# Performance work log

Hardware: AMD Instinct MI355X
Metric: run time of the kernel (lower is better)

## Reference

```python
import jax, jax.numpy as jnp
import numpy as np

REG = 0.01          # regularisation (target epsilon)
DECAY = 0.9         # decay_rate
MIN_UPDATE = 0.01   # min_update_size
MAX_ITERS = 50      # max_iterations
GRAD_CLIP = 1.0     # transport_gradient_clip
B, N, D = 4, 2048, 16


@jax.custom_vjp
def clip_grad_identity(t):
    # identity fwd; clips the cotangent of the transport matrix in bwd
    return t

def _cg_fwd(t):
    return t, None

def _cg_bwd(_, dt):
    return (jnp.clip(dt, -GRAD_CLIP, GRAD_CLIP),)

clip_grad_identity.defvjp(_cg_fwd, _cg_bwd)


def _diameter(x):
    # max over dims of per-sample std (ddof=0), per batch -> (B,1)
    d = jnp.max(jnp.std(x, axis=1), axis=-1, keepdims=True)
    return jnp.where(d == 0.0, jnp.ones_like(d), d)


def _sq_cdist(x):
    # squared euclidean auto-distance matrix, (B,N,N)
    sq = jnp.sum(x * x, axis=-1)
    c = sq[:, :, None] + sq[:, None, :] - 2.0 * jnp.einsum('bnd,bmd->bnm', x, x)
    return jnp.maximum(c, 0.0)


def sinkhorn_loop(log_a, log_b, cost, eps_target, min_update, max_iter, eps0, rate):
    """Log-domain Sinkhorn with per-batch exponentially decayed epsilon and
    masked early stopping (data-dependent stop expressed as a convergence mask
    so the loop is jit/vjp friendly). eps0: (B,1,1) initial regularisation
    (extent of the scaled particles, per Thornton & Corenflos)."""
    Bb, _ = log_a.shape
    init = (jnp.zeros_like(log_a), jnp.zeros_like(log_b), eps0,
            jnp.zeros((Bb, 1), dtype=bool))

    @jax.checkpoint
    def step(carry, _):
        f, g, eps, done = carry              # eps: (B,1,1), done: (B,1)
        eps2 = eps[:, :, 0]                  # (B,1)
        # f_i = -eps * LSE_j( log_b_j + (g_j - C_ij)/eps )
        f_new = -eps2 * jax.nn.logsumexp(log_b[:, None, :] + (g[:, None, :] - cost) / eps, axis=-1)
        cT = jnp.swapaxes(cost, 1, 2)
        # g_j = -eps * LSE_i( log_a_i + (f_i - C_ij)/eps )
        g_new = -eps2 * jax.nn.logsumexp(log_a[:, None, :] + (f_new[:, None, :] - cT) / eps, axis=-1)
        upd = jnp.maximum(jnp.max(jnp.abs(f_new - f), axis=-1),
                          jnp.max(jnp.abs(g_new - g), axis=-1))[:, None]  # (B,1)
        converged = (upd < min_update) & (eps2 <= eps_target)
        f = jnp.where(done, f, f_new)
        g = jnp.where(done, g, g_new)
        eps = jnp.where(done[:, :, None], eps, jnp.maximum(eps * rate, eps_target))
        done = done | converged
        return (f, g, eps, done), None

    (f, g, eps, _), _ = jax.lax.scan(step, init, None, length=max_iter)
    return f, g, eps


def _forward(state, weight):
    n = state.shape[1]
    log_b = jnp.full(weight.shape, -jnp.log(float(n)), weight.dtype)  # log uniform
    centred = state - jax.lax.stop_gradient(jnp.mean(state, axis=1, keepdims=True))
    scale = jax.lax.stop_gradient(_diameter(state)) * jnp.sqrt(float(state.shape[-1]))  # (B,1)
    sx = centred / scale[:, :, None]
    cost = _sq_cdist(sx)                                              # (B,N,N)
    extent = (jnp.max(sx, axis=(1, 2)) - jnp.min(sx, axis=(1, 2))).reshape(-1, 1, 1)
    f, g, _ = sinkhorn_loop(weight, log_b, cost, REG, MIN_UPDATE, MAX_ITERS, extent, DECAY)
    # transport from potentials at the target regularisation
    log_T = weight[:, :, None] + log_b[:, None, :] + (f[:, :, None] + g[:, None, :] - cost) / REG
    transport = clip_grad_identity(jnp.exp(log_T))                    # (B,N,N)
    # new particle m = N * sum_n T_nm x_n
    new_state = float(n) * jnp.einsum('bnm,bnd->bmd', transport, state)
    return new_state


def setup_inputs() -> dict:
    key = jax.random.key(0)
    k1, k2 = jax.random.split(key)
    state = jax.random.normal(k1, (B, N, D), dtype=jnp.float32)
    weight = jax.nn.log_softmax(jax.random.normal(k2, (B, N), dtype=jnp.float32), axis=-1)
    return {"state": state, "weight": weight}


def reference(state, weight):
    new_state = _forward(state, weight)
    uniform_log_w = jnp.full(weight.shape, -jnp.log(float(weight.shape[1])), weight.dtype)
    return (new_state, uniform_log_w)
```

## Files before the change

kernel.cpp:

```cpp
#include <hip/hip_runtime.h>

#define BATCH 4
#define NPTS  2048
#define DIM   16
#define REGEPS 0.01f
#define DECAYF 0.9f
#define MINUPD 0.01f
#define MAXIT  50
#define LOGN   7.62461898616f
#define L2E    1.44269504089f
#define LN2    0.69314718056f

#define OFF_SX    0
#define OFF_SQ    (BATCH*NPTS*DIM)
#define OFF_F     (OFF_SQ + BATCH*NPTS)
#define OFF_G     (OFF_F + BATCH*NPTS)
#define OFF_MEAN  (OFF_G + BATCH*NPTS)
#define OFF_SCALE (OFF_MEAN + BATCH*DIM)
#define OFF_EPS0  (OFF_SCALE + BATCH)
#define OFF_SYNC  155776

__global__ __launch_bounds__(256) void ot_preproc(const float* __restrict__ state,
                                                  float* __restrict__ ws) {
  const int b = blockIdx.x;
  const int tid = threadIdx.x;
  __shared__ float s_sum[16][17];
  __shared__ float s_sq[16][17];
  __shared__ float s_mean[16];
  __shared__ float s_red[8];
  __shared__ float s_scale_sh;

  const float* st = state + b * NPTS * DIM;
  const int d = tid & 15, grp = tid >> 4;
  float sm = 0.f, s2 = 0.f;
  for (int n = grp; n < NPTS; n += 16) {
    float x = st[n * DIM + d];
    sm += x; s2 += x * x;
  }
  s_sum[grp][d] = sm; s_sq[grp][d] = s2;
  __syncthreads();
  if (tid < 16) {
    float S = 0.f, Q = 0.f;
    for (int g2 = 0; g2 < 16; ++g2) { S += s_sum[g2][tid]; Q += s_sq[g2][tid]; }
    float mean = S * (1.0f / NPTS);
    float var  = fmaxf(Q * (1.0f / NPTS) - mean * mean, 0.f);
    float sd   = sqrtf(var);
    s_mean[tid] = mean;
    ws[OFF_MEAN + b * DIM + tid] = mean;
    s_sum[0][tid] = sd;
  }
  __syncthreads();
  if (tid == 0) {
    float dm = 0.f;
    for (int d2 = 0; d2 < 16; ++d2) dm = fmaxf(dm, s_sum[0][d2]);
    if (dm == 0.f) dm = 1.f;
    float scale = dm * 4.0f;
    s_scale_sh = scale;
    ws[OFF_SCALE + b] = scale;
  }
  __syncthreads();

  const float inv_scale = 1.0f / s_scale_sh;
  float vmin = 3.0e38f, vmax = -3.0e38f;
  float* sx = ws + OFF_SX + b * NPTS * DIM;
  float* sq = ws + OFF_SQ + b * NPTS;
  for (int n = tid; n < NPTS; n += 256) {
    const float4* rp = (const float4*)(st + n * DIM);
    float4 xs0 = rp[0], xs1 = rp[1], xs2 = rp[2], xs3 = rp[3];
    float xv[16] = {xs0.x,xs0.y,xs0.z,xs0.w, xs1.x,xs1.y,xs1.z,xs1.w,
                    xs2.x,xs2.y,xs2.z,xs2.w, xs3.x,xs3.y,xs3.z,xs3.w};
    float ov[16];
    float q = 0.f;
    #pragma unroll
    for (int e = 0; e < 16; ++e) {
      float v = (xv[e] - s_mean[e]) * inv_scale;
      ov[e] = v; q += v * v;
      vmin = fminf(vmin, v); vmax = fmaxf(vmax, v);
    }
    float4* op = (float4*)(sx + n * DIM);
    op[0] = make_float4(ov[0],ov[1],ov[2],ov[3]);
    op[1] = make_float4(ov[4],ov[5],ov[6],ov[7]);
    op[2] = make_float4(ov[8],ov[9],ov[10],ov[11]);
    op[3] = make_float4(ov[12],ov[13],ov[14],ov[15]);
    sq[n] = q;
  }
  float* fv = ws + OFF_F + b * NPTS;
  float* gv = ws + OFF_G + b * NPTS;
  for (int n = tid; n < NPTS; n += 256) { fv[n] = 0.f; gv[n] = 0.f; }
  #pragma unroll
  for (int off = 32; off > 0; off >>= 1) {
    vmin = fminf(vmin, __shfl_xor(vmin, off));
    vmax = fmaxf(vmax, __shfl_xor(vmax, off));
  }
  const int wv = tid >> 6, ln = tid & 63;
  if (ln == 0) { s_red[wv] = vmin; s_red[4 + wv] = vmax; }
  __syncthreads();
  if (tid == 0) {
    float mn = fminf(fminf(s_red[0], s_red[1]), fminf(s_red[2], s_red[3]));
    float mx = fmaxf(fmaxf(s_red[4], s_red[5]), fmaxf(s_red[6], s_red[7]));
    ws[OFF_EPS0 + b] = mx - mn;
    int* sy = (int*)ws + OFF_SYNC + b * 64;
    sy[0] = 0;
    ((unsigned int*)sy)[2] = 0u;
    ((unsigned int*)sy)[3] = 0u;
    sy[32] = 0;
  }
}

__device__ __forceinline__ float4 load_f4_coherent(const float* p) {
  float4 v;
  asm volatile("global_load_dwordx4 %0, %1, off sc0 sc1\n\t"
               "s_waitcnt vmcnt(0)"
               : "=v"(v) : "v"(p) : "memory");
  return v;
}

__device__ __forceinline__ void batch_barrier(int* sy, int ph) {
  __syncthreads();
  if (threadIdx.x == 0) {
    int* arrive = sy;
    int* epoch  = sy + 32;
    const int old = __hip_atomic_fetch_add(arrive, 1, __ATOMIC_ACQ_REL,
                                           __HIP_MEMORY_SCOPE_AGENT);
    if (old == 64 * ph - 1) {
      __hip_atomic_store(epoch, ph, __ATOMIC_RELEASE, __HIP_MEMORY_SCOPE_AGENT);
    } else {
      while (__hip_atomic_load(epoch, __ATOMIC_RELAXED, __HIP_MEMORY_SCOPE_AGENT) < ph)
        __builtin_amdgcn_s_sleep(2);
      (void)__hip_atomic_load(epoch, __ATOMIC_ACQUIRE, __HIP_MEMORY_SCOPE_AGENT);
    }
  }
  __syncthreads();
}

__device__ __forceinline__ void lse_sweep(const float* __restrict__ s_xt,
                                          const float* __restrict__ s_a2,
                                          const float (&sxs)[4][16],
                                          float (&M)[4], float (&S)[4], int l) {
  #pragma unroll
  for (int r = 0; r < 4; ++r) { M[r] = -3.0e38f; S[r] = 0.0f; }
  for (int c = 0; c < 8; ++c) {
    const int jb = c * 256 + 4 * l;
    const float4 av = *(const float4*)(s_a2 + jb);
    float acc[4][4];
    {
      const float4 xj = *(const float4*)(s_xt + jb);
      #pragma unroll
      for (int r = 0; r < 4; ++r) {
        acc[r][0] = fmaf(sxs[r][0], xj.x, av.x);
        acc[r][1] = fmaf(sxs[r][0], xj.y, av.y);
        acc[r][2] = fmaf(sxs[r][0], xj.z, av.z);
        acc[r][3] = fmaf(sxs[r][0], xj.w, av.w);
      }
    }
    #pragma unroll
    for (int dd = 1; dd < 16; ++dd) {
      const float4 xj = *(const float4*)(s_xt + dd * 2048 + jb);
      #pragma unroll
      for (int r = 0; r < 4; ++r) {
        acc[r][0] = fmaf(sxs[r][dd], xj.x, acc[r][0]);
        acc[r][1] = fmaf(sxs[r][dd], xj.y, acc[r][1]);
        acc[r][2] = fmaf(sxs[r][dd], xj.z, acc[r][2]);
        acc[r][3] = fmaf(sxs[r][dd], xj.w, acc[r][3]);
      }
    }
    #pragma unroll
    for (int r = 0; r < 4; ++r) {
      const float cmx = fmaxf(fmaxf(acc[r][0], acc[r][1]), fmaxf(acc[r][2], acc[r][3]));
      const float nm = fmaxf(M[r], cmx);
      const float e0 = exp2f(M[r] - nm);
      const float sa = exp2f(acc[r][0]-nm) + exp2f(acc[r][1]-nm)
                     + exp2f(acc[r][2]-nm) + exp2f(acc[r][3]-nm);
      S[r] = fmaf(S[r], e0, sa);
      M[r] = nm;
    }
  }
}

__device__ __forceinline__ void lse_butterfly(float (&M)[4], float (&S)[4]) {
  #pragma unroll
  for (int off = 1; off < 64; off <<= 1) {
    #pragma unroll
    for (int r = 0; r < 4; ++r) {
      const float om = __shfl_xor(M[r], off);
      const float os = __shfl_xor(S[r], off);
      const float nm = fmaxf(M[r], om);
      S[r] = S[r] * exp2f(M[r] - nm) + os * exp2f(om - nm);
      M[r] = nm;
    }
  }
}

__global__ __launch_bounds__(512, 2) void ot_sinkhorn(float* __restrict__ ws,
                                                      const float* __restrict__ wlog) {
  extern __shared__ float lds[];
  float* s_xt  = lds;
  float* s_a2  = lds + 16 * 2048;
  float* s_wl2 = s_a2 + 2048;

  const int bid = blockIdx.x;
  const int b  = bid >> 6;
  const int rb = bid & 63;
  const int tid = threadIdx.x;
  const int w = tid >> 6, l = tid & 63;

  const float* __restrict__ sx = ws + OFF_SX + b * NPTS * DIM;
  const float* __restrict__ sq = ws + OFF_SQ + b * NPTS;
  float* fv = ws + OFF_F + b * NPTS;
  float* gv = ws + OFF_G + b * NPTS;
  const float* __restrict__ wl = wlog + b * NPTS;
  int* sy = (int*)ws + OFF_SYNC + b * 64;
  unsigned int* up2 = (unsigned int*)sy + 2;

  for (int j = tid; j < NPTS; j += 512) {
    const float4* rp = (const float4*)(sx + j * DIM);
    float4 t0 = rp[0], t1 = rp[1], t2 = rp[2], t3 = rp[3];
    s_xt[ 0*2048+j]=t0.x; s_xt[ 1*2048+j]=t0.y; s_xt[ 2*2048+j]=t0.z; s_xt[ 3*2048+j]=t0.w;
    s_xt[ 4*2048+j]=t1.x; s_xt[ 5*2048+j]=t1.y; s_xt[ 6*2048+j]=t1.z; s_xt[ 7*2048+j]=t1.w;
    s_xt[ 8*2048+j]=t2.x; s_xt[ 9*2048+j]=t2.y; s_xt[10*2048+j]=t2.z; s_xt[11*2048+j]=t2.w;
    s_xt[12*2048+j]=t3.x; s_xt[13*2048+j]=t3.y; s_xt[14*2048+j]=t3.z; s_xt[15*2048+j]=t3.w;
    s_wl2[j] = wl[j] * L2E;
  }
  const int row0 = rb * 32 + w * 4;
  float sxs[4][16];
  #pragma unroll
  for (int r = 0; r < 4; ++r) {
    const float4* rp = (const float4*)(sx + (row0 + r) * DIM);
    float4 t0 = rp[0], t1 = rp[1], t2 = rp[2], t3 = rp[3];
    sxs[r][0]=t0.x;  sxs[r][1]=t0.y;  sxs[r][2]=t0.z;  sxs[r][3]=t0.w;
    sxs[r][4]=t1.x;  sxs[r][5]=t1.y;  sxs[r][6]=t1.z;  sxs[r][7]=t1.w;
    sxs[r][8]=t2.x;  sxs[r][9]=t2.y;  sxs[r][10]=t2.z; sxs[r][11]=t2.w;
    sxs[r][12]=t3.x; sxs[r][13]=t3.y; sxs[r][14]=t3.z; sxs[r][15]=t3.w;
  }
  float eps = ws[OFF_EPS0 + b];
  {
    const float s2e0 = 2.0f * L2E / eps;
    #pragma unroll
    for (int r = 0; r < 4; ++r)
      #pragma unroll
      for (int dd = 0; dd < 16; ++dd) sxs[r][dd] *= s2e0;
  }
  __syncthreads();

  int ph = 0;
  for (int it = 0; it < MAXIT; ++it) {
    const float le   = L2E / eps;
    const float eln2 = eps * LN2;

    {
      const int j4 = tid * 4;
      const float4 gj = load_f4_coherent(gv + j4);
      const float4 qj = *(const float4*)(sq + j4);
      *(float4*)(s_a2 + j4) = make_float4((gj.x - qj.x) * le, (gj.y - qj.y) * le,
                                          (gj.z - qj.z) * le, (gj.w - qj.w) * le);
    }
    __syncthreads();
    {
      float M[4], S[4];
      lse_sweep(s_xt, s_a2, sxs, M, S, l);
      lse_butterfly(M, S);
      if (l < 4) {
        const float Mr = (l==0)?M[0]:(l==1)?M[1]:(l==2)?M[2]:M[3];
        const float Sr = (l==0)?S[0]:(l==1)?S[1]:(l==2)?S[2]:S[3];
        const int i = row0 + l;
        const float qi = sq[i];
        const float fnew = fmaf(eps, LOGN, qi) - eln2 * (Mr + log2f(Sr));
        const float old = __hip_atomic_load(fv + i, __ATOMIC_RELAXED, __HIP_MEMORY_SCOPE_AGENT);
        __hip_atomic_store(fv + i, fnew, __ATOMIC_RELEASE, __HIP_MEMORY_SCOPE_AGENT);
        __hip_atomic_fetch_max(up2 + (it & 1), __float_as_uint(fabsf(fnew - old)),
                               __ATOMIC_RELAXED, __HIP_MEMORY_SCOPE_AGENT);
      }
    }
    ++ph; batch_barrier(sy, ph);

    if (rb == 0 && tid == 0)
      __hip_atomic_store(up2 + ((it + 1) & 1), 0u, __ATOMIC_RELAXED, __HIP_MEMORY_SCOPE_AGENT);
    {
      const int j4 = tid * 4;
      const float4 fj = load_f4_coherent(fv + j4);
      const float4 qj = *(const float4*)(sq + j4);
      const float4 w2 = *(const float4*)(s_wl2 + j4);
      *(float4*)(s_a2 + j4) = make_float4(fmaf(fj.x - qj.x, le, w2.x), fmaf(fj.y - qj.y, le, w2.y),
                                          fmaf(fj.z - qj.z, le, w2.z), fmaf(fj.w - qj.w, le, w2.w));
    }
    __syncthreads();
    {
      float M[4], S[4];
      lse_sweep(s_xt, s_a2, sxs, M, S, l);
      lse_butterfly(M, S);
      if (l < 4) {
        const float Mr = (l==0)?M[0]:(l==1)?M[1]:(l==2)?M[2]:M[3];
        const float Sr = (l==0)?S[0]:(l==1)?S[1]:(l==2)?S[2]:S[3];
        const int i = row0 + l;
        const float qm = sq[i];
        const float gnew = qm - eln2 * (Mr + log2f(Sr));
        const float old = __hip_atomic_load(gv + i, __ATOMIC_RELAXED, __HIP_MEMORY_SCOPE_AGENT);
        __hip_atomic_store(gv + i, gnew, __ATOMIC_RELEASE, __HIP_MEMORY_SCOPE_AGENT);
        __hip_atomic_fetch_max(up2 + (it & 1), __float_as_uint(fabsf(gnew - old)),
                               __ATOMIC_RELAXED, __HIP_MEMORY_SCOPE_AGENT);
      }
    }
    if (it < MAXIT - 1) {
      ++ph; batch_barrier(sy, ph);
      const unsigned uu = __hip_atomic_load(up2 + (it & 1), __ATOMIC_RELAXED, __HIP_MEMORY_SCOPE_AGENT);
      const bool conv = (__uint_as_float(uu) < MINUPD) && (eps <= REGEPS);
      if (conv) break;
      const float en = fmaxf(eps * DECAYF, REGEPS);
      const float ratio = eps / en;
      eps = en;
      #pragma unroll
      for (int r = 0; r < 4; ++r)
        #pragma unroll
        for (int dd = 0; dd < 16; ++dd) sxs[r][dd] *= ratio;
    }
  }
}

__global__ __launch_bounds__(256) void ot_out(float* __restrict__ ws,
                                              const float* __restrict__ wlog,
                                              float* __restrict__ out) {
  __shared__ float s_xt[DIM][256];
  __shared__ float s_p[256];
  __shared__ float s_q[256];
  const int bid = blockIdx.x;
  const int b  = bid >> 8;
  const int rb = bid & 255;
  const int tid = threadIdx.x;
  const int w = tid >> 6, l = tid & 63;
  const float invR = 1.0f / REGEPS;

  const float* __restrict__ sx = ws + OFF_SX + b * NPTS * DIM;
  const float* __restrict__ sq = ws + OFF_SQ + b * NPTS;
  const float* __restrict__ fv = ws + OFF_F + b * NPTS;
  const float* __restrict__ gv = ws + OFF_G + b * NPTS;
  const float* __restrict__ wl = wlog + b * NPTS;

  const int row0 = rb * 8 + w * 2;
  float sxm[2][DIM], cm2[2], qm[2], acc[2][DIM], accT[2];
  #pragma unroll
  for (int r = 0; r < 2; ++r) {
    const int mrow = row0 + r;
    cm2[r] = sq[mrow];
    qm[r]  = gv[mrow] * invR;
    const float4* rp = (const float4*)(sx + mrow * DIM);
    #pragma unroll
    for (int c4 = 0; c4 < 4; ++c4) {
      float4 t = rp[c4];
      sxm[r][c4*4+0] = -2.0f * t.x; sxm[r][c4*4+1] = -2.0f * t.y;
      sxm[r][c4*4+2] = -2.0f * t.z; sxm[r][c4*4+3] = -2.0f * t.w;
    }
    #pragma unroll
    for (int dd = 0; dd < DIM; ++dd) acc[r][dd] = 0.0f;
    accT[r] = 0.0f;
  }

  for (int k = 0; k < NPTS / 256; ++k) {
    __syncthreads();
    {
      const int n = k * 256 + tid;
      const float4* rp = (const float4*)(sx + n * DIM);
      float4 t0 = rp[0], t1 = rp[1], t2 = rp[2], t3 = rp[3];
      s_xt[0][tid]=t0.x;  s_xt[1][tid]=t0.y;  s_xt[2][tid]=t0.z;  s_xt[3][tid]=t0.w;
      s_xt[4][tid]=t1.x;  s_xt[5][tid]=t1.y;  s_xt[6][tid]=t1.z;  s_xt[7][tid]=t1.w;
      s_xt[8][tid]=t2.x;  s_xt[9][tid]=t2.y;  s_xt[10][tid]=t2.z; s_xt[11][tid]=t2.w;
      s_xt[12][tid]=t3.x; s_xt[13][tid]=t3.y; s_xt[14][tid]=t3.z; s_xt[15][tid]=t3.w;
      s_q[tid] = sq[n];
      s_p[tid] = wl[n] - LOGN + fv[n] * invR;
    }
    __syncthreads();
    const float4 pv = *(const float4*)&s_p[4 * l];
    const float4 qv = *(const float4*)&s_q[4 * l];
    float a2[2][4];
    #pragma unroll
    for (int r = 0; r < 2; ++r) {
      a2[r][0] = cm2[r] + qv.x; a2[r][1] = cm2[r] + qv.y;
      a2[r][2] = cm2[r] + qv.z; a2[r][3] = cm2[r] + qv.w;
    }
    #pragma unroll
    for (int dd = 0; dd < DIM; ++dd) {
      const float4 xj = *(const float4*)&s_xt[dd][4 * l];
      #pragma unroll
      for (int r = 0; r < 2; ++r) {
        const float xr = sxm[r][dd];
        a2[r][0] = fmaf(xr, xj.x, a2[r][0]);
        a2[r][1] = fmaf(xr, xj.y, a2[r][1]);
        a2[r][2] = fmaf(xr, xj.z, a2[r][2]);
        a2[r][3] = fmaf(xr, xj.w, a2[r][3]);
      }
    }
    float T[2][4];
    #pragma unroll
    for (int r = 0; r < 2; ++r) {
      T[r][0] = __expf(fmaf(fmaxf(a2[r][0], 0.f), -invR, pv.x + qm[r]));
      T[r][1] = __expf(fmaf(fmaxf(a2[r][1], 0.f), -invR, pv.y + qm[r]));
      T[r][2] = __expf(fmaf(fmaxf(a2[r][2], 0.f), -invR, pv.z + qm[r]));
      T[r][3] = __expf(fmaf(fmaxf(a2[r][3], 0.f), -invR, pv.w + qm[r]));
      accT[r] += (T[r][0] + T[r][1]) + (T[r][2] + T[r][3]);
    }
    #pragma unroll
    for (int dd = 0; dd < DIM; ++dd) {
      const float4 xj = *(const float4*)&s_xt[dd][4 * l];
      #pragma unroll
      for (int r = 0; r < 2; ++r) {
        float t = acc[r][dd];
        t = fmaf(T[r][0], xj.x, t);
        t = fmaf(T[r][1], xj.y, t);
        t = fmaf(T[r][2], xj.z, t);
        t = fmaf(T[r][3], xj.w, t);
        acc[r][dd] = t;
      }
    }
  }
  #pragma unroll
  for (int off = 1; off < 64; off <<= 1) {
    #pragma unroll
    for (int r = 0; r < 2; ++r) {
      #pragma unroll
      for (int dd = 0; dd < DIM; ++dd) acc[r][dd] += __shfl_xor(acc[r][dd], off);
      accT[r] += __shfl_xor(accT[r], off);
    }
  }
  if (l == 0) {
    const float scale = ws[OFF_SCALE + b];
    const float* mean = ws + OFF_MEAN + b * DIM;
    #pragma unroll
    for (int r = 0; r < 2; ++r) {
      const int mrow = row0 + r;
      float ov[16];
      #pragma unroll
      for (int dd = 0; dd < DIM; ++dd)
        ov[dd] = (float)NPTS * fmaf(scale, acc[r][dd], mean[dd] * accT[r]);
      float4* op = (float4*)(out + (b * NPTS + mrow) * DIM);
      op[0] = make_float4(ov[0],ov[1],ov[2],ov[3]);
      op[1] = make_float4(ov[4],ov[5],ov[6],ov[7]);
      op[2] = make_float4(ov[8],ov[9],ov[10],ov[11]);
      op[3] = make_float4(ov[12],ov[13],ov[14],ov[15]);
    }
  }
  if (tid < 8) out[BATCH * NPTS * DIM + b * NPTS + rb * 8 + tid] = -LOGN;
}

extern "C" void kernel_launch(void* const* d_in, const int* in_sizes, int n_in,
                              void* d_out, int out_size, void* d_ws, size_t ws_size,
                              hipStream_t stream) {
  (void)in_sizes; (void)n_in; (void)out_size; (void)ws_size;
  const float* state  = (const float*)d_in[0];
  const float* weight = (const float*)d_in[1];
  float* out = (float*)d_out;
  float* ws  = (float*)d_ws;

  ot_preproc<<<dim3(BATCH), dim3(256), 0, stream>>>(state, ws);

  const unsigned int dynLds = 147456;
  hipFuncSetAttribute((const void*)ot_sinkhorn,
                      hipFuncAttributeMaxDynamicSharedMemorySize, (int)dynLds);
  hipLaunchKernelGGL(ot_sinkhorn, dim3(256), dim3(512), dynLds, stream, ws, weight);

  ot_out<<<dim3(BATCH * NPTS / 8), dim3(256), 0, stream>>>(ws, weight, out);
}
```

Before: 3.311 ms.

## Split Sinkhorn LSE column sweep across two wave groups with LDS merge

Doubles the Sinkhorn block to 1024 threads so two groups of waves each sweep half of the columns for the same rows, then merges the partial max/sum pairs through a small LDS buffer. Row coordinates become wave-uniform (readfirstlane) and unscaled by epsilon, with 1/eps applied at the end of each tile instead of rescaling 64 registers per iteration. This aims to raise parallelism and latency hiding per CU, at the cost of an extra __syncthreads and merge step per half-iteration and more register pressure under the 1024-thread launch bound.

Result: no change. 3.364 ms (+1.6%).

```diff
diff --git a/kernel.cpp b/kernel.cpp
--- a/kernel.cpp
+++ b/kernel.cpp
@@ -133,24 +133,29 @@
   __syncthreads();
 }
 
-__device__ __forceinline__ void lse_sweep(const float* __restrict__ s_xt,
-                                          const float* __restrict__ s_a2,
-                                          const float (&sxs)[4][16],
-                                          float (&M)[4], float (&S)[4], int l) {
+__device__ __forceinline__ float rfl(float v) {
+  return __int_as_float(__builtin_amdgcn_readfirstlane(__float_as_int(v)));
+}
+
+__device__ __forceinline__ void lse_sweep_half(const float* __restrict__ s_xt,
+                                               const float* __restrict__ s_a2,
+                                               const float (&sxr)[4][16],
+                                               float inv_eps, int jbase, int l,
+                                               float (&M)[4], float (&S)[4]) {
   #pragma unroll
   for (int r = 0; r < 4; ++r) { M[r] = -3.0e38f; S[r] = 0.0f; }
-  for (int c = 0; c < 8; ++c) {
-    const int jb = c * 256 + 4 * l;
+  for (int c = 0; c < 4; ++c) {
+    const int jb = jbase + c * 256 + 4 * l;
     const float4 av = *(const float4*)(s_a2 + jb);
     float acc[4][4];
     {
       const float4 xj = *(const float4*)(s_xt + jb);
       #pragma unroll
       for (int r = 0; r < 4; ++r) {
-        acc[r][0] = fmaf(sxs[r][0], xj.x, av.x);
-        acc[r][1] = fmaf(sxs[r][0], xj.y, av.y);
-        acc[r][2] = fmaf(sxs[r][0], xj.z, av.z);
-        acc[r][3] = fmaf(sxs[r][0], xj.w, av.w);
+        acc[r][0] = sxr[r][0] * xj.x;
+        acc[r][1] = sxr[r][0] * xj.y;
+        acc[r][2] = sxr[r][0] * xj.z;
+        acc[r][3] = sxr[r][0] * xj.w;
       }
     }
     #pragma unroll
@@ -158,19 +163,22 @@
       const float4 xj = *(const float4*)(s_xt + dd * 2048 + jb);
       #pragma unroll
       for (int r = 0; r < 4; ++r) {
-        acc[r][0] = fmaf(sxs[r][dd], xj.x, acc[r][0]);
-        acc[r][1] = fmaf(sxs[r][dd], xj.y, acc[r][1]);
-        acc[r][2] = fmaf(sxs[r][dd], xj.z, acc[r][2]);
-        acc[r][3] = fmaf(sxs[r][dd], xj.w, acc[r][3]);
+        acc[r][0] = fmaf(sxr[r][dd], xj.x, acc[r][0]);
+        acc[r][1] = fmaf(sxr[r][dd], xj.y, acc[r][1]);
+        acc[r][2] = fmaf(sxr[r][dd], xj.z, acc[r][2]);
+        acc[r][3] = fmaf(sxr[r][dd], xj.w, acc[r][3]);
       }
     }
     #pragma unroll
     for (int r = 0; r < 4; ++r) {
-      const float cmx = fmaxf(fmaxf(acc[r][0], acc[r][1]), fmaxf(acc[r][2], acc[r][3]));
+      const float v0 = fmaf(acc[r][0], inv_eps, av.x);
+      const float v1 = fmaf(acc[r][1], inv_eps, av.y);
+      const float v2 = fmaf(acc[r][2], inv_eps, av.z);
+      const float v3 = fmaf(acc[r][3], inv_eps, av.w);
+      const float cmx = fmaxf(fmaxf(v0, v1), fmaxf(v2, v3));
       const float nm = fmaxf(M[r], cmx);
       const float e0 = exp2f(M[r] - nm);
-      const float sa = exp2f(acc[r][0]-nm) + exp2f(acc[r][1]-nm)
-                     + exp2f(acc[r][2]-nm) + exp2f(acc[r][3]-nm);
+      const float sa = exp2f(v0-nm) + exp2f(v1-nm) + exp2f(v2-nm) + exp2f(v3-nm);
       S[r] = fmaf(S[r], e0, sa);
       M[r] = nm;
     }
@@ -191,18 +199,21 @@
   }
 }
 
-__global__ __launch_bounds__(512, 2) void ot_sinkhorn(float* __restrict__ ws,
-                                                      const float* __restrict__ wlog) {
+__global__ __launch_bounds__(1024, 4) void ot_sinkhorn(float* __restrict__ ws,
+                                                       const float* __restrict__ wlog) {
   extern __shared__ float lds[];
   float* s_xt  = lds;
   float* s_a2  = lds + 16 * 2048;
   float* s_wl2 = s_a2 + 2048;
+  float* s_mrg = s_wl2 + 2048;
 
   const int bid = blockIdx.x;
   const int b  = bid >> 6;
   const int rb = bid & 63;
   const int tid = threadIdx.x;
   const int w = tid >> 6, l = tid & 63;
+  const int wlo = w & 7;
+  const int jbase = (w >> 3) * 1024;
 
   const float* __restrict__ sx = ws + OFF_SX + b * NPTS * DIM;
   const float* __restrict__ sq = ws + OFF_SQ + b * NPTS;
@@ -212,7 +223,7 @@
   int* sy = (int*)ws + OFF_SYNC + b * 64;
   unsigned int* up2 = (unsigned int*)sy + 2;
 
-  for (int j = tid; j < NPTS; j += 512) {
+  for (int j = tid; j < NPTS; j += 1024) {
     const float4* rp = (const float4*)(sx + j * DIM);
     float4 t0 = rp[0], t1 = rp[1], t2 = rp[2], t3 = rp[3];
     s_xt[ 0*2048+j]=t0.x; s_xt[ 1*2048+j]=t0.y; s_xt[ 2*2048+j]=t0.z; s_xt[ 3*2048+j]=t0.w;
@@ -221,33 +232,28 @@
     s_xt[12*2048+j]=t3.x; s_xt[13*2048+j]=t3.y; s_xt[14*2048+j]=t3.z; s_xt[15*2048+j]=t3.w;
     s_wl2[j] = wl[j] * L2E;
   }
-  const int row0 = rb * 32 + w * 4;
-  float sxs[4][16];
+  const int row0 = rb * 32 + wlo * 4;
+  float sxr[4][16];
   #pragma unroll
   for (int r = 0; r < 4; ++r) {
     const float4* rp = (const float4*)(sx + (row0 + r) * DIM);
-    float4 t0 = rp[0], t1 = rp[1], t2 = rp[2], t3 = rp[3];
-    sxs[r][0]=t0.x;  sxs[r][1]=t0.y;  sxs[r][2]=t0.z;  sxs[r][3]=t0.w;
-    sxs[r][4]=t1.x;  sxs[r][5]=t1.y;  sxs[r][6]=t1.z;  sxs[r][7]=t1.w;
-    sxs[r][8]=t2.x;  sxs[r][9]=t2.y;  sxs[r][10]=t2.z; sxs[r][11]=t2.w;
-    sxs[r][12]=t3.x; sxs[r][13]=t3.y; sxs[r][14]=t3.z; sxs[r][15]=t3.w;
+    const float4 t0 = rp[0], t1 = rp[1], t2 = rp[2], t3 = rp[3];
+    const float c2 = 2.0f * L2E;
+    sxr[r][0]=rfl(t0.x*c2);  sxr[r][1]=rfl(t0.y*c2);  sxr[r][2]=rfl(t0.z*c2);  sxr[r][3]=rfl(t0.w*c2);
+    sxr[r][4]=rfl(t1.x*c2);  sxr[r][5]=rfl(t1.y*c2);  sxr[r][6]=rfl(t1.z*c2);  sxr[r][7]=rfl(t1.w*c2);
+    sxr[r][8]=rfl(t2.x*c2);  sxr[r][9]=rfl(t2.y*c2);  sxr[r][10]=rfl(t2.z*c2); sxr[r][11]=rfl(t2.w*c2);
+    sxr[r][12]=rfl(t3.x*c2); sxr[r][13]=rfl(t3.y*c2); sxr[r][14]=rfl(t3.z*c2); sxr[r][15]=rfl(t3.w*c2);
   }
   float eps = ws[OFF_EPS0 + b];
-  {
-    const float s2e0 = 2.0f * L2E / eps;
-    #pragma unroll
-    for (int r = 0; r < 4; ++r)
-      #pragma unroll
-      for (int dd = 0; dd < 16; ++dd) sxs[r][dd] *= s2e0;
-  }
   __syncthreads();
 
   int ph = 0;
   for (int it = 0; it < MAXIT; ++it) {
-    const float le   = L2E / eps;
-    const float eln2 = eps * LN2;
-
-    {
+    const float le      = L2E / eps;
+    const float eln2    = eps * LN2;
+    const float inv_eps = 1.0f / eps;
+
+    if (tid < 512) {
       const int j4 = tid * 4;
       const float4 gj = load_f4_coherent(gv + j4);
       const float4 qj = *(const float4*)(sq + j4);
@@ -257,14 +263,25 @@
     __syncthreads();
     {
       float M[4], S[4];
-      lse_sweep(s_xt, s_a2, sxs, M, S, l);
+      lse_sweep_half(s_xt, s_a2, sxr, inv_eps, jbase, l, M, S);
       lse_butterfly(M, S);
-      if (l < 4) {
+      if (w >= 8 && l < 4) {
         const float Mr = (l==0)?M[0]:(l==1)?M[1]:(l==2)?M[2]:M[3];
         const float Sr = (l==0)?S[0]:(l==1)?S[1]:(l==2)?S[2]:S[3];
+        s_mrg[(wlo * 4 + l) * 2]     = Mr;
+        s_mrg[(wlo * 4 + l) * 2 + 1] = Sr;
+      }
+      __syncthreads();
+      if (w < 8 && l < 4) {
+        const float M1 = (l==0)?M[0]:(l==1)?M[1]:(l==2)?M[2]:M[3];
+        const float S1 = (l==0)?S[0]:(l==1)?S[1]:(l==2)?S[2]:S[3];
+        const float M2 = s_mrg[(wlo * 4 + l) * 2];
+        const float S2 = s_mrg[(wlo * 4 + l) * 2 + 1];
+        const float nm = fmaxf(M1, M2);
+        const float St = S1 * exp2f(M1 - nm) + S2 * exp2f(M2 - nm);
         const int i = row0 + l;
         const float qi = sq[i];
-        const float fnew = fmaf(eps, LOGN, qi) - eln2 * (Mr + log2f(Sr));
+        const float fnew = fmaf(eps, LOGN, qi) - eln2 * (nm + log2f(St));
         const float old = __hip_atomic_load(fv + i, __ATOMIC_RELAXED, __HIP_MEMORY_SCOPE_AGENT);
         __hip_atomic_store(fv + i, fnew, __ATOMIC_RELEASE, __HIP_MEMORY_SCOPE_AGENT);
         __hip_atomic_fetch_max(up2 + (it & 1), __float_as_uint(fabsf(fnew - old)),
@@ -275,7 +292,7 @@
 
     if (rb == 0 && tid == 0)
       __hip_atomic_store(up2 + ((it + 1) & 1), 0u, __ATOMIC_RELAXED, __HIP_MEMORY_SCOPE_AGENT);
-    {
+    if (tid < 512) {
       const int j4 = tid * 4;
       const float4 fj = load_f4_coherent(fv + j4);
       const float4 qj = *(const float4*)(sq + j4);
@@ -286,14 +303,25 @@
     __syncthreads();
     {
       float M[4], S[4];
-      lse_sweep(s_xt, s_a2, sxs, M, S, l);
+      lse_sweep_half(s_xt, s_a2, sxr, inv_eps, jbase, l, M, S);
       lse_butterfly(M, S);
-      if (l < 4) {
+      if (w >= 8 && l < 4) {
         const float Mr = (l==0)?M[0]:(l==1)?M[1]:(l==2)?M[2]:M[3];
         const float Sr = (l==0)?S[0]:(l==1)?S[1]:(l==2)?S[2]:S[3];
+        s_mrg[(wlo * 4 + l) * 2]     = Mr;
+        s_mrg[(wlo * 4 + l) * 2 + 1] = Sr;
+      }
+      __syncthreads();
+      if (w < 8 && l < 4) {
+        const float M1 = (l==0)?M[0]:(l==1)?M[1]:(l==2)?M[2]:M[3];
+        const float S1 = (l==0)?S[0]:(l==1)?S[1]:(l==2)?S[2]:S[3];
+        const float M2 = s_mrg[(wlo * 4 + l) * 2];
+        const float S2 = s_mrg[(wlo * 4 + l) * 2 + 1];
+        const float nm = fmaxf(M1, M2);
+        const float St = S1 * exp2f(M1 - nm) + S2 * exp2f(M2 - nm);
         const int i = row0 + l;
         const float qm = sq[i];
-        const float gnew = qm - eln2 * (Mr + log2f(Sr));
+        const float gnew = qm - eln2 * (nm + log2f(St));
         const float old = __hip_atomic_load(gv + i, __ATOMIC_RELAXED, __HIP_MEMORY_SCOPE_AGENT);
         __hip_atomic_store(gv + i, gnew, __ATOMIC_RELEASE, __HIP_MEMORY_SCOPE_AGENT);
         __hip_atomic_fetch_max(up2 + (it & 1), __float_as_uint(fabsf(gnew - old)),
@@ -305,13 +333,7 @@
       const unsigned uu = __hip_atomic_load(up2 + (it & 1), __ATOMIC_RELAXED, __HIP_MEMORY_SCOPE_AGENT);
       const bool conv = (__uint_as_float(uu) < MINUPD) && (eps <= REGEPS);
       if (conv) break;
-      const float en = fmaxf(eps * DECAYF, REGEPS);
-      const float ratio = eps / en;
-      eps = en;
-      #pragma unroll
-      for (int r = 0; r < 4; ++r)
-        #pragma unroll
-        for (int dd = 0; dd < 16; ++dd) sxs[r][dd] *= ratio;
+      eps = fmaxf(eps * DECAYF, REGEPS);
     }
   }
 }
@@ -451,10 +473,10 @@
 
   ot_preproc<<<dim3(BATCH), dim3(256), 0, stream>>>(state, ws);
 
-  const unsigned int dynLds = 147456;
+  const unsigned int dynLds = 147712;
   hipFuncSetAttribute((const void*)ot_sinkhorn,
                       hipFuncAttributeMaxDynamicSharedMemorySize, (int)dynLds);
-  hipLaunchKernelGGL(ot_sinkhorn, dim3(256), dim3(512), dynLds, stream, ws, weight);
+  hipLaunchKernelGGL(ot_sinkhorn, dim3(256), dim3(1024), dynLds, stream, ws, weight);
 
   ot_out<<<dim3(BATCH * NPTS / 8), dim3(256), 0, stream>>>(ws, weight, out);
 }
```

## Replace atomic-counter barrier with flag array, packed-FMA sweep, local update reduction

Applied to the files above, without the earlier changes.

Replaces the per-batch atomic fetch-add grid barrier with per-block flag stores that block 0 polls through a wavefront ballot before publishing an epoch. The convergence max is now reduced inside each block and issued as a single atomic per block rather than one per row. The row-feature registers are reloaded from LDS every iteration, and 1/eps is applied after the dot product using packed two-wide FMAs. Squared norms are cached in LDS. The aim is to shorten barrier latency and cut atomic traffic and register pressure, at the cost of extra LDS reads and a slightly different rounding order.

After: 4.316 ms. 1.3x slower.

```diff
diff --git a/kernel.cpp b/kernel.cpp
--- a/kernel.cpp
+++ b/kernel.cpp
@@ -10,6 +10,8 @@
 #define LOGN   7.62461898616f
 #define L2E    1.44269504089f
 #define LN2    0.69314718056f
+
+typedef float v2f __attribute__((ext_vector_type(2)));
 
 #define OFF_SX    0
 #define OFF_SQ    (BATCH*NPTS*DIM)
@@ -99,12 +101,9 @@
     float mn = fminf(fminf(s_red[0], s_red[1]), fminf(s_red[2], s_red[3]));
     float mx = fmaxf(fmaxf(s_red[4], s_red[5]), fmaxf(s_red[6], s_red[7]));
     ws[OFF_EPS0 + b] = mx - mn;
-    int* sy = (int*)ws + OFF_SYNC + b * 64;
-    sy[0] = 0;
-    ((unsigned int*)sy)[2] = 0u;
-    ((unsigned int*)sy)[3] = 0u;
-    sy[32] = 0;
-  }
+  }
+  int* sy = (int*)ws + OFF_SYNC + b * 128;
+  for (int k = tid; k < 128; k += 256) sy[k] = 0;
 }
 
 __device__ __forceinline__ float4 load_f4_coherent(const float* p) {
@@ -115,19 +114,25 @@
   return v;
 }
 
-__device__ __forceinline__ void batch_barrier(int* sy, int ph) {
-  __syncthreads();
-  if (threadIdx.x == 0) {
-    int* arrive = sy;
-    int* epoch  = sy + 32;
-    const int old = __hip_atomic_fetch_add(arrive, 1, __ATOMIC_ACQ_REL,
-                                           __HIP_MEMORY_SCOPE_AGENT);
-    if (old == 64 * ph - 1) {
-      __hip_atomic_store(epoch, ph, __ATOMIC_RELEASE, __HIP_MEMORY_SCOPE_AGENT);
-    } else {
+__device__ __forceinline__ void batch_barrier(int* flags, int* epoch, int rb, int ph) {
+  __syncthreads();
+  const int tid = threadIdx.x;
+  if (tid < 64) {
+    if (tid == 0)
+      __hip_atomic_store(flags + rb, ph, __ATOMIC_RELEASE, __HIP_MEMORY_SCOPE_AGENT);
+    if (rb == 0) {
+      for (;;) {
+        const int v = __hip_atomic_load(flags + tid, __ATOMIC_RELAXED, __HIP_MEMORY_SCOPE_AGENT);
+        if (__ballot(v >= ph) == 0xFFFFFFFFFFFFFFFFull) break;
+        __builtin_amdgcn_s_sleep(4);
+      }
+      __threadfence();
+      if (tid == 0)
+        __hip_atomic_store(epoch, ph, __ATOMIC_RELEASE, __HIP_MEMORY_SCOPE_AGENT);
+    } else if (tid == 0) {
       while (__hip_atomic_load(epoch, __ATOMIC_RELAXED, __HIP_MEMORY_SCOPE_AGENT) < ph)
-        __builtin_amdgcn_s_sleep(2);
-      (void)__hip_atomic_load(epoch, __ATOMIC_ACQUIRE, __HIP_MEMORY_SCOPE_AGENT);
+        __builtin_amdgcn_s_sleep(4);
+      __threadfence();
     }
   }
   __syncthreads();
@@ -135,42 +140,47 @@
 
 __device__ __forceinline__ void lse_sweep(const float* __restrict__ s_xt,
                                           const float* __restrict__ s_a2,
-                                          const float (&sxs)[4][16],
-                                          float (&M)[4], float (&S)[4], int l) {
+                                          const float (&sxr)[4][16],
+                                          float inv_eps, int l,
+                                          float (&M)[4], float (&S)[4]) {
+  const v2f inv2 = { inv_eps, inv_eps };
   #pragma unroll
   for (int r = 0; r < 4; ++r) { M[r] = -3.0e38f; S[r] = 0.0f; }
   for (int c = 0; c < 8; ++c) {
     const int jb = c * 256 + 4 * l;
-    const float4 av = *(const float4*)(s_a2 + jb);
-    float acc[4][4];
-    {
-      const float4 xj = *(const float4*)(s_xt + jb);
+    const v2f* a2v = (const v2f*)(s_a2 + jb);
+    const v2f av0 = a2v[0], av1 = a2v[1];
+    v2f acc[4][2];
+    {
+      const v2f* xv = (const v2f*)(s_xt + jb);
+      const v2f x0 = xv[0], x1 = xv[1];
       #pragma unroll
       for (int r = 0; r < 4; ++r) {
-        acc[r][0] = fmaf(sxs[r][0], xj.x, av.x);
-        acc[r][1] = fmaf(sxs[r][0], xj.y, av.y);
-        acc[r][2] = fmaf(sxs[r][0], xj.z, av.z);
-        acc[r][3] = fmaf(sxs[r][0], xj.w, av.w);
+        const v2f sv = { sxr[r][0], sxr[r][0] };
+        acc[r][0] = x0 * sv;
+        acc[r][1] = x1 * sv;
       }
     }
     #pragma unroll
     for (int dd = 1; dd < 16; ++dd) {
-      const float4 xj = *(const float4*)(s_xt + dd * 2048 + jb);
+      const v2f* xv = (const v2f*)(s_xt + dd * 2048 + jb);
+      const v2f x0 = xv[0], x1 = xv[1];
       #pragma unroll
       for (int r = 0; r < 4; ++r) {
-        acc[r][0] = fmaf(sxs[r][dd], xj.x, acc[r][0]);
-        acc[r][1] = fmaf(sxs[r][dd], xj.y, acc[r][1]);
-        acc[r][2] = fmaf(sxs[r][dd], xj.z, acc[r][2]);
-        acc[r][3] = fmaf(sxs[r][dd], xj.w, acc[r][3]);
+        const v2f sv = { sxr[r][dd], sxr[r][dd] };
+        acc[r][0] = __builtin_elementwise_fma(x0, sv, acc[r][0]);
+        acc[r][1] = __builtin_elementwise_fma(x1, sv, acc[r][1]);
       }
     }
     #pragma unroll
     for (int r = 0; r < 4; ++r) {
-      const float cmx = fmaxf(fmaxf(acc[r][0], acc[r][1]), fmaxf(acc[r][2], acc[r][3]));
+      const v2f v01 = __builtin_elementwise_fma(acc[r][0], inv2, av0);
+      const v2f v23 = __builtin_elementwise_fma(acc[r][1], inv2, av1);
+      const float v0 = v01.x, v1 = v01.y, v2 = v23.x, v3 = v23.y;
+      const float cmx = fmaxf(fmaxf(v0, v1), fmaxf(v2, v3));
       const float nm = fmaxf(M[r], cmx);
       const float e0 = exp2f(M[r] - nm);
-      const float sa = exp2f(acc[r][0]-nm) + exp2f(acc[r][1]-nm)
-                     + exp2f(acc[r][2]-nm) + exp2f(acc[r][3]-nm);
+      const float sa = exp2f(v0-nm) + exp2f(v1-nm) + exp2f(v2-nm) + exp2f(v3-nm);
       S[r] = fmaf(S[r], e0, sa);
       M[r] = nm;
     }
@@ -197,6 +207,8 @@
   float* s_xt  = lds;
   float* s_a2  = lds + 16 * 2048;
   float* s_wl2 = s_a2 + 2048;
+  float* s_q   = s_wl2 + 2048;
+  float* s_red = s_q + 2048;
 
   const int bid = blockIdx.x;
   const int b  = bid >> 6;
@@ -209,8 +221,10 @@
   float* fv = ws + OFF_F + b * NPTS;
   float* gv = ws + OFF_G + b * NPTS;
   const float* __restrict__ wl = wlog + b * NPTS;
-  int* sy = (int*)ws + OFF_SYNC + b * 64;
-  unsigned int* up2 = (unsigned int*)sy + 2;
+  int* sy    = (int*)ws + OFF_SYNC + b * 128;
+  int* flags = sy;
+  int* epoch = sy + 64;
+  unsigned int* up2 = (unsigned int*)sy + 66;
 
   for (int j = tid; j < NPTS; j += 512) {
     const float4* rp = (const float4*)(sx + j * DIM);
@@ -220,98 +234,107 @@
     s_xt[ 8*2048+j]=t2.x; s_xt[ 9*2048+j]=t2.y; s_xt[10*2048+j]=t2.z; s_xt[11*2048+j]=t2.w;
     s_xt[12*2048+j]=t3.x; s_xt[13*2048+j]=t3.y; s_xt[14*2048+j]=t3.z; s_xt[15*2048+j]=t3.w;
     s_wl2[j] = wl[j] * L2E;
+    s_q[j]   = sq[j];
   }
   const int row0 = rb * 32 + w * 4;
-  float sxs[4][16];
-  #pragma unroll
-  for (int r = 0; r < 4; ++r) {
-    const float4* rp = (const float4*)(sx + (row0 + r) * DIM);
-    float4 t0 = rp[0], t1 = rp[1], t2 = rp[2], t3 = rp[3];
-    sxs[r][0]=t0.x;  sxs[r][1]=t0.y;  sxs[r][2]=t0.z;  sxs[r][3]=t0.w;
-    sxs[r][4]=t1.x;  sxs[r][5]=t1.y;  sxs[r][6]=t1.z;  sxs[r][7]=t1.w;
-    sxs[r][8]=t2.x;  sxs[r][9]=t2.y;  sxs[r][10]=t2.z; sxs[r][11]=t2.w;
-    sxs[r][12]=t3.x; sxs[r][13]=t3.y; sxs[r][14]=t3.z; sxs[r][15]=t3.w;
-  }
+  const float qi_own = (l < 4) ? sq[row0 + l] : 0.f;
+  float fprev = 0.f, gprev = 0.f;
   float eps = ws[OFF_EPS0 + b];
-  {
-    const float s2e0 = 2.0f * L2E / eps;
-    #pragma unroll
-    for (int r = 0; r < 4; ++r)
-      #pragma unroll
-      for (int dd = 0; dd < 16; ++dd) sxs[r][dd] *= s2e0;
-  }
   __syncthreads();
 
   int ph = 0;
   for (int it = 0; it < MAXIT; ++it) {
-    const float le   = L2E / eps;
-    const float eln2 = eps * LN2;
+    const float le      = L2E / eps;
+    const float eln2    = eps * LN2;
+    const float inv_eps = 1.0f / eps;
+
+    float sxr[4][16];
+    {
+      const volatile float* vxt = s_xt;
+      #pragma unroll
+      for (int r = 0; r < 4; ++r)
+        #pragma unroll
+        for (int dd = 0; dd < 16; ++dd)
+          sxr[r][dd] = vxt[dd * 2048 + row0 + r] * (2.0f * L2E);
+    }
 
     {
       const int j4 = tid * 4;
-      const float4 gj = load_f4_coherent(gv + j4);
-      const float4 qj = *(const float4*)(sq + j4);
-      *(float4*)(s_a2 + j4) = make_float4((gj.x - qj.x) * le, (gj.y - qj.y) * le,
-                                          (gj.z - qj.z) * le, (gj.w - qj.w) * le);
-    }
-    __syncthreads();
+      const float4 g4 = load_f4_coherent(gv + j4);
+      const float4 q4 = *(const float4*)(s_q + j4);
+      *(float4*)(s_a2 + j4) = make_float4((g4.x - q4.x) * le, (g4.y - q4.y) * le,
+                                          (g4.z - q4.z) * le, (g4.w - q4.w) * le);
+    }
+    __syncthreads();
+    float updv = 0.f;
     {
       float M[4], S[4];
-      lse_sweep(s_xt, s_a2, sxs, M, S, l);
+      lse_sweep(s_xt, s_a2, sxr, inv_eps, l, M, S);
       lse_butterfly(M, S);
       if (l < 4) {
         const float Mr = (l==0)?M[0]:(l==1)?M[1]:(l==2)?M[2]:M[3];
         const float Sr = (l==0)?S[0]:(l==1)?S[1]:(l==2)?S[2]:S[3];
-        const int i = row0 + l;
-        const float qi = sq[i];
-        const float fnew = fmaf(eps, LOGN, qi) - eln2 * (Mr + log2f(Sr));
-        const float old = __hip_atomic_load(fv + i, __ATOMIC_RELAXED, __HIP_MEMORY_SCOPE_AGENT);
-        __hip_atomic_store(fv + i, fnew, __ATOMIC_RELEASE, __HIP_MEMORY_SCOPE_AGENT);
-        __hip_atomic_fetch_max(up2 + (it & 1), __float_as_uint(fabsf(fnew - old)),
-                               __ATOMIC_RELAXED, __HIP_MEMORY_SCOPE_AGENT);
-      }
-    }
-    ++ph; batch_barrier(sy, ph);
+        const float fnew = fmaf(eps, LOGN, qi_own) - eln2 * (Mr + log2f(Sr));
+        __hip_atomic_store(fv + row0 + l, fnew, __ATOMIC_RELEASE, __HIP_MEMORY_SCOPE_AGENT);
+        updv = fabsf(fnew - fprev);
+        fprev = fnew;
+      }
+      updv = fmaxf(updv, __shfl_xor(updv, 1));
+      updv = fmaxf(updv, __shfl_xor(updv, 2));
+      if (l == 0) s_red[w] = updv;
+    }
+    __syncthreads();
+    if (tid == 0) {
+      float u = s_red[0];
+      #pragma unroll
+      for (int k = 1; k < 8; ++k) u = fmaxf(u, s_red[k]);
+      __hip_atomic_fetch_max(up2 + (it & 1), __float_as_uint(u),
+                             __ATOMIC_RELAXED, __HIP_MEMORY_SCOPE_AGENT);
+    }
+    ++ph; batch_barrier(flags, epoch, rb, ph);
 
     if (rb == 0 && tid == 0)
       __hip_atomic_store(up2 + ((it + 1) & 1), 0u, __ATOMIC_RELAXED, __HIP_MEMORY_SCOPE_AGENT);
     {
       const int j4 = tid * 4;
-      const float4 fj = load_f4_coherent(fv + j4);
-      const float4 qj = *(const float4*)(sq + j4);
+      const float4 f4 = load_f4_coherent(fv + j4);
+      const float4 q4 = *(const float4*)(s_q + j4);
       const float4 w2 = *(const float4*)(s_wl2 + j4);
-      *(float4*)(s_a2 + j4) = make_float4(fmaf(fj.x - qj.x, le, w2.x), fmaf(fj.y - qj.y, le, w2.y),
-                                          fmaf(fj.z - qj.z, le, w2.z), fmaf(fj.w - qj.w, le, w2.w));
-    }
-    __syncthreads();
+      *(float4*)(s_a2 + j4) = make_float4(fmaf(f4.x - q4.x, le, w2.x), fmaf(f4.y - q4.y, le, w2.y),
+                                          fmaf(f4.z - q4.z, le, w2.z), fmaf(f4.w - q4.w, le, w2.w));
+    }
+    __syncthreads();
+    updv = 0.f;
     {
       float M[4], S[4];
-      lse_sweep(s_xt, s_a2, sxs, M, S, l);
+      lse_sweep(s_xt, s_a2, sxr, inv_eps, l, M, S);
       lse_butterfly(M, S);
       if (l < 4) {
         const float Mr = (l==0)?M[0]:(l==1)?M[1]:(l==2)?M[2]:M[3];
         const float Sr = (l==0)?S[0]:(l==1)?S[1]:(l==2)?S[2]:S[3];
-        const int i = row0 + l;
-        const float qm = sq[i];
-        const float gnew = qm - eln2 * (Mr + log2f(Sr));
-        const float old = __hip_atomic_load(gv + i, __ATOMIC_RELAXED, __HIP_MEMORY_SCOPE_AGENT);
-        __hip_atomic_store(gv + i, gnew, __ATOMIC_RELEASE, __HIP_MEMORY_SCOPE_AGENT);
-        __hip_atomic_fetch_max(up2 + (it & 1), __float_as_uint(fabsf(gnew - old)),
-                               __ATOMIC_RELAXED, __HIP_MEMORY_SCOPE_AGENT);
-      }
+        const float gnew = qi_own - eln2 * (Mr + log2f(Sr));
+        __hip_atomic_store(gv + row0 + l, gnew, __ATOMIC_RELEASE, __HIP_MEMORY_SCOPE_AGENT);
+        updv = fabsf(gnew - gprev);
+        gprev = gnew;
+      }
+      updv = fmaxf(updv, __shfl_xor(updv, 1));
+      updv = fmaxf(updv, __shfl_xor(updv, 2));
+      if (l == 0) s_red[w] = updv;
+    }
+    __syncthreads();
+    if (tid == 0) {
+      float u = s_red[0];
+      #pragma unroll
+      for (int k = 1; k < 8; ++k) u = fmaxf(u, s_red[k]);
+      __hip_atomic_fetch_max(up2 + (it & 1), __float_as_uint(u),
+                             __ATOMIC_RELAXED, __HIP_MEMORY_SCOPE_AGENT);
     }
     if (it < MAXIT - 1) {
-      ++ph; batch_barrier(sy, ph);
+      ++ph; batch_barrier(flags, epoch, rb, ph);
       const unsigned uu = __hip_atomic_load(up2 + (it & 1), __ATOMIC_RELAXED, __HIP_MEMORY_SCOPE_AGENT);
       const bool conv = (__uint_as_float(uu) < MINUPD) && (eps <= REGEPS);
       if (conv) break;
-      const float en = fmaxf(eps * DECAYF, REGEPS);
-      const float ratio = eps / en;
-      eps = en;
-      #pragma unroll
-      for (int r = 0; r < 4; ++r)
-        #pragma unroll
-        for (int dd = 0; dd < 16; ++dd) sxs[r][dd] *= ratio;
+      eps = fmaxf(eps * DECAYF, REGEPS);
     }
   }
 }
@@ -451,9 +474,9 @@
 
   ot_preproc<<<dim3(BATCH), dim3(256), 0, stream>>>(state, ws);
 
-  const unsigned int dynLds = 147456;
-  hipFuncSetAttribute((const void*)ot_sinkhorn,
-                      hipFuncAttributeMaxDynamicSharedMemorySize, (int)dynLds);
+  const unsigned int dynLds = (16 * 2048 + 3 * 2048 + 8) * 4;
+  (void)hipFuncSetAttribute((const void*)ot_sinkhorn,
+                            hipFuncAttributeMaxDynamicSharedMemorySize, (int)dynLds);
   hipLaunchKernelGGL(ot_sinkhorn, dim3(256), dim3(512), dynLds, stream, ws, weight);
 
   ot_out<<<dim3(BATCH * NPTS / 8), dim3(256), 0, stream>>>(ws, weight, out);
```
